# Kernel optimization log

Measured on AMD Instinct MI355X. Metric: run time of the kernel, lower is better.

The kernel has to match this reference:

```python
import jax, jax.numpy as jnp
import numpy as np
from math import sqrt

EPS = 1e-8


def setup_inputs() -> dict:
    rng = jax.random.key(0)
    k1, k2, k3 = jax.random.split(rng, 3)
    BS, NA, NB, NK, NV = 16, 2048, 2048, 64, 64
    key = jax.random.normal(k1, (BS, NA, 1, NK), dtype=jnp.float32)
    query = jax.random.normal(k2, (BS, 1, NB, NK), dtype=jnp.float32)
    value = jax.random.normal(k3, (BS, NA, NV), dtype=jnp.float32)
    return {"key": key, "query": query, "value": value}


def reference(key, query, value):
    # key: (BS, NA, 1, NK); query: (BS, 1, NB, NK); value: (BS, NA, NV)
    NK = key.shape[-1]
    NV = value.shape[-1]
    BS, NB = query.shape[0], query.shape[2]
    # weights = sum(key * query, 3) / sqrt(NK)  -> (BS, NA, NB), via einsum
    w = jnp.einsum('bak,bnk->ban', key[:, :, 0, :], query[:, 0, :, :]) / sqrt(NK)
    # softmax over NA (dim 1), beta=1, drop=False
    w = jax.nn.softmax(w, axis=1)
    # values = sum_a w[b,a,n] * value[b,a,v] -> (BS, NB, NV)
    vals = jnp.einsum('ban,bav->bnv', w, value)
    # norm over feature dim (torch.std is unbiased, ddof=1)
    v2 = vals.reshape(BS * NB, NV)
    mu = v2.mean(axis=1, keepdims=True)
    std = v2.std(axis=1, keepdims=True, ddof=1)
    v2 = (v2 - mu) / (std + EPS)
    out = v2.reshape(BS, NB, NV).transpose(0, 2, 1)  # (BS, NV, NB)
    return out, w
```

## Files before the change

kernel.cpp:

```cpp
#include <hip/hip_runtime.h>
#include <math.h>

#define BS 16
#define NA 2048
#define NB 2048
#define NK 64
#define NV 64
#define EPS 1e-8f

typedef float        f32x4  __attribute__((ext_vector_type(4)));
typedef __bf16       bf16x8 __attribute__((ext_vector_type(8)));
typedef short        s16x8  __attribute__((ext_vector_type(8)));
typedef unsigned int u32x4  __attribute__((ext_vector_type(4)));
typedef unsigned short u16x8 __attribute__((ext_vector_type(8)));

template <typename V>
__device__ __forceinline__ auto mfma_impl(V a, V b, f32x4 c, int)
    -> decltype(__builtin_amdgcn_mfma_f32_16x16x32_bf16(a, b, c, 0, 0, 0)) {
    return __builtin_amdgcn_mfma_f32_16x16x32_bf16(a, b, c, 0, 0, 0);
}
template <typename V>
__device__ __forceinline__ auto mfma_impl(V a, V b, f32x4 c, long)
    -> decltype(__builtin_amdgcn_mfma_f32_16x16x32_bf16(
           __builtin_bit_cast(s16x8, a), __builtin_bit_cast(s16x8, b), c, 0, 0, 0)) {
    return __builtin_amdgcn_mfma_f32_16x16x32_bf16(
        __builtin_bit_cast(s16x8, a), __builtin_bit_cast(s16x8, b), c, 0, 0, 0);
}
__device__ __forceinline__ f32x4 mfma_bf16(u32x4 a, u32x4 b, f32x4 c) {
    bf16x8 av = __builtin_bit_cast(bf16x8, a);
    bf16x8 bv = __builtin_bit_cast(bf16x8, b);
    return mfma_impl(av, bv, c, 0);
}

__device__ __forceinline__ unsigned short f2bf(float x) {
    unsigned u = __builtin_bit_cast(unsigned, x);
    unsigned r = (u + 0x7FFFu + ((u >> 16) & 1u)) >> 16;
    return (unsigned short)r;
}
__device__ __forceinline__ u16x8 pk8(f32x4 a, f32x4 b) {
    u16x8 p;
    p[0] = f2bf(a[0]); p[1] = f2bf(a[1]); p[2] = f2bf(a[2]); p[3] = f2bf(a[3]);
    p[4] = f2bf(b[0]); p[5] = f2bf(b[1]); p[6] = f2bf(b[2]); p[7] = f2bf(b[3]);
    return p;
}
__device__ __forceinline__ f32x4 ldg4(const float* p) { return *(const f32x4*)p; }

__device__ __forceinline__ void bar_lgkm() {
    asm volatile("s_waitcnt lgkmcnt(0)" ::: "memory");
    __builtin_amdgcn_s_barrier();
}

__device__ __forceinline__ int swz128(int lin) {
    const int r = lin >> 7;
    const int c16 = (lin >> 4) & 7;
    return (r << 7) + ((c16 ^ (r & 7)) << 4) + (lin & 15);
}

__global__ __launch_bounds__(256)
void conv_k_kernel(const float* __restrict__ key, unsigned short* __restrict__ kb) {
    size_t i = ((size_t)blockIdx.x * 256 + threadIdx.x) * 8;
    f32x4 a = *(const f32x4*)(key + i);
    f32x4 b = *(const f32x4*)(key + i + 4);
    *(u16x8*)(kb + i) = pk8(a, b);
}

__global__ __launch_bounds__(256)
void transpose_v_kernel(const float* __restrict__ v, unsigned short* __restrict__ vt) {
    __shared__ float tile[64][65];
    const int b = blockIdx.y, at = blockIdx.x * 64;
    const float* Vb = v + (size_t)b * NA * NV;
    unsigned short* Vtb = vt + (size_t)b * NV * NA;
    const int r = threadIdx.x >> 2, c = (threadIdx.x & 3) * 16;
    #pragma unroll
    for (int j = 0; j < 4; ++j)
        *(f32x4*)&tile[r][c + 4 * j] = ldg4(Vb + (size_t)(at + r) * NV + c + 4 * j);
    __syncthreads();
    u16x8 p0, p1;
    #pragma unroll
    for (int j = 0; j < 8; ++j) p0[j] = f2bf(tile[c + j][r]);
    #pragma unroll
    for (int j = 0; j < 8; ++j) p1[j] = f2bf(tile[c + 8 + j][r]);
    *(u16x8*)(Vtb + (size_t)r * NA + at + c) = p0;
    *(u16x8*)(Vtb + (size_t)r * NA + at + c + 8) = p1;
}

#define BN2 32
#define NT  32
#define KD0 0
#define KD1 8192
#define VD0 16384
#define VD1 24576
#define ESB 32768
#define LRED 36864
#define LINV 37376
#define SMEMSZ 37504

__global__ __launch_bounds__(256, 4)
void attn_main7_kernel(const unsigned short* __restrict__ kb,
                       const float* __restrict__ qf,
                       const unsigned short* __restrict__ vtb,
                       float* __restrict__ out,
                       float* __restrict__ wout)
{
    __shared__ __align__(16) char smem[SMEMSZ];
    const int tid = threadIdx.x, w = tid >> 6, lane = tid & 63;
    const int lr = lane & 15, lg = lane >> 4;

    const int lin = blockIdx.x;
    const int swz = (lin & 7) * 128 + (lin >> 3);
    const int b = swz >> 6, nb = (swz & 63) * BN2;

    const char* Kb = (const char*)(kb + (size_t)b * NA * NK);
    const char* Vt = (const char*)(vtb + (size_t)b * NV * NA);
    const float* Qb = qf + (size_t)b * NB * NK;
    float* Wb = wout + (size_t)b * NA * NB;
    float* Ob = out + (size_t)b * NV * NB;

    u32x4 af[2][2];
    #pragma unroll
    for (int t = 0; t < 2; ++t)
        #pragma unroll
        for (int c = 0; c < 2; ++c) {
            const float* qp = Qb + (size_t)(nb + t * 16 + lr) * NK + c * 32 + lg * 8;
            f32x4 qa = ldg4(qp);
            f32x4 qb2 = ldg4(qp + 4);
            af[t][c] = __builtin_bit_cast(u32x4, pk8(qa, qb2));
        }

    const int lin0 = tid * 16;
    const int lin1 = tid * 16 + 4096;
    const int kdst0 = swz128(lin0), kdst1 = swz128(lin1);
    const int vsrc0 = ((lin0 >> 7) * (NA * 2)) + (lin0 & 127);
    const int vsrc1 = ((lin1 >> 7) * (NA * 2)) + (lin1 & 127);

    const int row = w * 16 + lr;
    int kfro[2];
    #pragma unroll
    for (int c = 0; c < 2; ++c)
        kfro[c] = row * 128 + (((c * 4 + lg) ^ (row & 7)) << 4);
    int esro[2][2];
    #pragma unroll
    for (int t = 0; t < 2; ++t)
        #pragma unroll
        for (int c = 0; c < 2; ++c) {
            const int rr = t * 16 + lr;
            esro[t][c] = rr * 128 + (((c * 4 + lg) ^ (rr & 7)) << 4);
        }
    int eswo[2][4];
    #pragma unroll
    for (int t = 0; t < 2; ++t)
        #pragma unroll
        for (int r = 0; r < 4; ++r) {
            const int n = t * 16 + lg * 4 + r;
            eswo[t][r] = n * 128 + (((w * 2 + (lr >> 3)) ^ (n & 7)) << 4) + (lr & 7) * 2;
        }

    u32x4 kr0 = *(const u32x4*)(Kb + lin0);
    u32x4 kr1 = *(const u32x4*)(Kb + lin1);
    *(u32x4*)(smem + KD0 + kdst0) = kr0;
    *(u32x4*)(smem + KD0 + kdst1) = kr1;
    bar_lgkm();

    float lacc[2][4] = {};
    for (int i = 0; i < NT; ++i) {
        const int p = i & 1;
        if (i + 1 < NT) {
            kr0 = *(const u32x4*)(Kb + (i + 1) * 8192 + lin0);
            kr1 = *(const u32x4*)(Kb + (i + 1) * 8192 + lin1);
        }
        const char* kbuf = smem + (p ? KD1 : KD0);
        u32x4 kf0 = *(const u32x4*)(kbuf + kfro[0]);
        u32x4 kf1 = *(const u32x4*)(kbuf + kfro[1]);
        #pragma unroll
        for (int t = 0; t < 2; ++t) {
            f32x4 acc = {0.f, 0.f, 0.f, 0.f};
            acc = mfma_bf16(af[t][0], kf0, acc);
            acc = mfma_bf16(af[t][1], kf1, acc);
            #pragma unroll
            for (int r = 0; r < 4; ++r)
                lacc[t][r] += __expf(acc[r] * 0.125f);
        }
        if (i + 1 < NT) {
            char* kbn = smem + (p ? KD0 : KD1);
            *(u32x4*)(kbn + kdst0) = kr0;
            *(u32x4*)(kbn + kdst1) = kr1;
        }
        bar_lgkm();
    }

    #pragma unroll
    for (int t = 0; t < 2; ++t)
        #pragma unroll
        for (int r = 0; r < 4; ++r) {
            float v = lacc[t][r];
            v += __shfl_xor(v, 1); v += __shfl_xor(v, 2);
            v += __shfl_xor(v, 4); v += __shfl_xor(v, 8);
            lacc[t][r] = v;
        }
    if (lr == 0) {
        float* lp = (float*)(smem + LRED);
        #pragma unroll
        for (int t = 0; t < 2; ++t)
            #pragma unroll
            for (int r = 0; r < 4; ++r)
                lp[w * 32 + t * 16 + lg * 4 + r] = lacc[t][r];
    }
    __syncthreads();
    if (tid < 32) {
        const float* lp = (const float*)(smem + LRED);
        ((float*)(smem + LINV))[tid] =
            1.0f / (lp[tid] + lp[32 + tid] + lp[64 + tid] + lp[96 + tid]);
    }
    __syncthreads();
    f32x4 linv[2];
    linv[0] = *(const f32x4*)(smem + LINV + (lg * 4) * 4);
    linv[1] = *(const f32x4*)(smem + LINV + (16 + lg * 4) * 4);

    f32x4 pacc[2] = {{0.f,0.f,0.f,0.f},{0.f,0.f,0.f,0.f}};

    kr0 = *(const u32x4*)(Kb + lin0);
    kr1 = *(const u32x4*)(Kb + lin1);
    u32x4 vr0 = *(const u32x4*)(Vt + vsrc0);
    u32x4 vr1 = *(const u32x4*)(Vt + vsrc1);
    *(u32x4*)(smem + KD0 + kdst0) = kr0;
    *(u32x4*)(smem + KD0 + kdst1) = kr1;
    *(u32x4*)(smem + VD0 + kdst0) = vr0;
    *(u32x4*)(smem + VD0 + kdst1) = vr1;
    bar_lgkm();

    for (int i = 0; i < NT; ++i) {
        const int p = i & 1;
        if (i + 1 < NT) {
            kr0 = *(const u32x4*)(Kb + (i + 1) * 8192 + lin0);
            kr1 = *(const u32x4*)(Kb + (i + 1) * 8192 + lin1);
            vr0 = *(const u32x4*)(Vt + (i + 1) * 128 + vsrc0);
            vr1 = *(const u32x4*)(Vt + (i + 1) * 128 + vsrc1);
        }
        const char* kbuf = smem + (p ? KD1 : KD0);
        const char* vbuf = smem + (p ? VD1 : VD0);
        u32x4 kf0 = *(const u32x4*)(kbuf + kfro[0]);
        u32x4 kf1 = *(const u32x4*)(kbuf + kfro[1]);
        const int at = i * 64;
        #pragma unroll
        for (int t = 0; t < 2; ++t) {
            f32x4 acc = {0.f, 0.f, 0.f, 0.f};
            acc = mfma_bf16(af[t][0], kf0, acc);
            acc = mfma_bf16(af[t][1], kf1, acc);
            f32x4 wv;
            #pragma unroll
            for (int r = 0; r < 4; ++r)
                wv[r] = __expf(acc[r] * 0.125f) * linv[t][r];
            *(f32x4*)(Wb + (size_t)(at + row) * NB + nb + t * 16 + lg * 4) = wv;
            #pragma unroll
            for (int r = 0; r < 4; ++r)
                *(unsigned short*)(smem + ESB + eswo[t][r]) = f2bf(wv[r]);
        }
        bar_lgkm();

        u32x4 pa[2][2];
        #pragma unroll
        for (int t = 0; t < 2; ++t)
            #pragma unroll
            for (int c = 0; c < 2; ++c)
                pa[t][c] = *(const u32x4*)(smem + ESB + esro[t][c]);
        u32x4 vf0 = *(const u32x4*)(vbuf + kfro[0]);
        u32x4 vf1 = *(const u32x4*)(vbuf + kfro[1]);
        #pragma unroll
        for (int t = 0; t < 2; ++t) {
            pacc[t] = mfma_bf16(pa[t][0], vf0, pacc[t]);
            pacc[t] = mfma_bf16(pa[t][1], vf1, pacc[t]);
        }
        if (i + 1 < NT) {
            char* kbn = smem + (p ? KD0 : KD1);
            char* vbn = smem + (p ? VD0 : VD1);
            *(u32x4*)(kbn + kdst0) = kr0;
            *(u32x4*)(kbn + kdst1) = kr1;
            *(u32x4*)(vbn + kdst0) = vr0;
            *(u32x4*)(vbn + kdst1) = vr1;
        }
        bar_lgkm();
    }

    __syncthreads();
    float* vals = (float*)smem;
    #pragma unroll
    for (int t = 0; t < 2; ++t)
        #pragma unroll
        for (int r = 0; r < 4; ++r)
            vals[(t * 16 + lg * 4 + r) * 66 + w * 16 + lr] = pacc[t][r];
    __syncthreads();
    {
        const int n = tid >> 3, v0 = (tid & 7) * 8;
        float sv[8], s1 = 0.f, s2 = 0.f;
        #pragma unroll
        for (int j = 0; j < 8; ++j) {
            float x = vals[n * 66 + v0 + j];
            sv[j] = x; s1 += x; s2 = fmaf(x, x, s2);
        }
        s1 += __shfl_xor(s1, 1); s2 += __shfl_xor(s2, 1);
        s1 += __shfl_xor(s1, 2); s2 += __shfl_xor(s2, 2);
        s1 += __shfl_xor(s1, 4); s2 += __shfl_xor(s2, 4);
        const float mu = s1 * (1.0f / 64.0f);
        float var = (s2 - 64.0f * mu * mu) * (1.0f / 63.0f);
        var = fmaxf(var, 0.0f);
        const float istd = 1.0f / (sqrtf(var) + EPS);
        #pragma unroll
        for (int j = 0; j < 8; ++j)
            vals[n * 66 + v0 + j] = (sv[j] - mu) * istd;
    }
    __syncthreads();
    {
        const int v = tid >> 2, q = (tid & 3) * 8;
        f32x4 o0, o1;
        #pragma unroll
        for (int j = 0; j < 4; ++j) o0[j] = vals[(q + j) * 66 + v];
        #pragma unroll
        for (int j = 0; j < 4; ++j) o1[j] = vals[(q + 4 + j) * 66 + v];
        *(f32x4*)(Ob + (size_t)v * NB + nb + q) = o0;
        *(f32x4*)(Ob + (size_t)v * NB + nb + q + 4) = o1;
    }
}

#define SQ 72
#define OSTR 68
#define SMEM_BYTES 38144

__global__ __launch_bounds__(256, 2)
void attn_fb_kernel(const float* __restrict__ key, const float* __restrict__ query,
                    const float* __restrict__ value, float* __restrict__ out,
                    float* __restrict__ wout)
{
    __shared__ __align__(16) char smem[SMEM_BYTES];
    unsigned short* Qs = (unsigned short*)(smem);
    unsigned short* Ks = (unsigned short*)(smem + 9216);
    unsigned short* Vts = (unsigned short*)(smem + 18432);
    unsigned short* Es = (unsigned short*)(smem + 27648);
    float* linv_s = (float*)(smem + 36864);
    float (*lred)[64] = (float (*)[64])(smem + 37120);
    float* outl = (float*)(smem + 18432);

    const int tid = threadIdx.x, wave = tid >> 6, lane = tid & 63;
    const int lr = lane & 15, lg = lane >> 4;
    const int b = blockIdx.y, nb = blockIdx.x * 64, aw = wave * 16;

    const float* Kb = key + (size_t)b * NA * NK;
    const float* Qb = query + (size_t)b * NB * NK;
    const float* Vb = value + (size_t)b * NA * NV;
    float* Wb = wout + (size_t)b * NA * NB;
    float* Ob = out + (size_t)b * NV * NB;

    {
        const int r = tid >> 2, c = (tid & 3) * 16;
        const float* src = Qb + (size_t)(nb + r) * NK + c;
        f32x4 q0 = ldg4(src), q1 = ldg4(src + 4), q2 = ldg4(src + 8), q3 = ldg4(src + 12);
        *(u16x8*)&Qs[r * SQ + c] = pk8(q0, q1);
        *(u16x8*)&Qs[r * SQ + c + 8] = pk8(q2, q3);
    }
    float lacc[4][4] = {};
    for (int at = 0; at < NA; at += 64) {
        {
            const int r = tid >> 2, c = (tid & 3) * 16;
            const float* src = Kb + (size_t)(at + r) * NK + c;
            f32x4 k0 = ldg4(src), k1 = ldg4(src + 4), k2 = ldg4(src + 8), k3 = ldg4(src + 12);
            *(u16x8*)&Ks[r * SQ + c] = pk8(k0, k1);
            *(u16x8*)&Ks[r * SQ + c + 8] = pk8(k2, k3);
        }
        __syncthreads();
        u32x4 bf0 = *(const u32x4*)&Ks[(aw + lr) * SQ + (lg * 8)];
        u32x4 bf1 = *(const u32x4*)&Ks[(aw + lr) * SQ + (32 + lg * 8)];
        #pragma unroll
        for (int t = 0; t < 4; ++t) {
            f32x4 acc = {0.f, 0.f, 0.f, 0.f};
            u32x4 af0 = *(const u32x4*)&Qs[(t * 16 + lr) * SQ + (lg * 8)];
            u32x4 af1 = *(const u32x4*)&Qs[(t * 16 + lr) * SQ + (32 + lg * 8)];
            acc = mfma_bf16(af0, bf0, acc);
            acc = mfma_bf16(af1, bf1, acc);
            #pragma unroll
            for (int r = 0; r < 4; ++r) lacc[t][r] += __expf(acc[r] * 0.125f);
        }
        __syncthreads();
    }
    #pragma unroll
    for (int t = 0; t < 4; ++t)
        #pragma unroll
        for (int r = 0; r < 4; ++r) {
            float v = lacc[t][r];
            v += __shfl_xor(v, 1); v += __shfl_xor(v, 2);
            v += __shfl_xor(v, 4); v += __shfl_xor(v, 8);
            lacc[t][r] = v;
        }
    if (lr == 0)
        #pragma unroll
        for (int t = 0; t < 4; ++t)
            #pragma unroll
            for (int r = 0; r < 4; ++r)
                lred[wave][t * 16 + lg * 4 + r] = lacc[t][r];
    __syncthreads();
    if (tid < 64) {
        float s = lred[0][tid] + lred[1][tid] + lred[2][tid] + lred[3][tid];
        linv_s[tid] = 1.0f / s;
    }
    __syncthreads();
    f32x4 linv[4];
    #pragma unroll
    for (int t = 0; t < 4; ++t) linv[t] = *(const f32x4*)&linv_s[t * 16 + lg * 4];

    f32x4 pacc[4] = {{0.f,0.f,0.f,0.f},{0.f,0.f,0.f,0.f},{0.f,0.f,0.f,0.f},{0.f,0.f,0.f,0.f}};
    for (int at = 0; at < NA; at += 64) {
        {
            const int r = tid >> 2, c = (tid & 3) * 16;
            const float* src = Kb + (size_t)(at + r) * NK + c;
            f32x4 k0 = ldg4(src), k1 = ldg4(src + 4), k2 = ldg4(src + 8), k3 = ldg4(src + 12);
            *(u16x8*)&Ks[r * SQ + c] = pk8(k0, k1);
            *(u16x8*)&Ks[r * SQ + c + 8] = pk8(k2, k3);
        }
        {
            const int ap = (tid & 31) * 2, q = tid >> 5;
            const float* v0p = Vb + (size_t)(at + ap) * NV + q * 8;
            const float* v1p = v0p + NV;
            f32x4 a0 = ldg4(v0p), a1 = ldg4(v0p + 4);
            f32x4 b0 = ldg4(v1p), b1 = ldg4(v1p + 4);
            #pragma unroll
            for (int j = 0; j < 4; ++j) {
                unsigned int w0 = (unsigned)f2bf(a0[j]) | ((unsigned)f2bf(b0[j]) << 16);
                *(unsigned int*)&Vts[(q * 8 + j) * SQ + ap] = w0;
                unsigned int w1 = (unsigned)f2bf(a1[j]) | ((unsigned)f2bf(b1[j]) << 16);
                *(unsigned int*)&Vts[(q * 8 + 4 + j) * SQ + ap] = w1;
            }
        }
        __syncthreads();
        u32x4 bf0 = *(const u32x4*)&Ks[(aw + lr) * SQ + (lg * 8)];
        u32x4 bf1 = *(const u32x4*)&Ks[(aw + lr) * SQ + (32 + lg * 8)];
        #pragma unroll
        for (int t = 0; t < 4; ++t) {
            f32x4 acc = {0.f, 0.f, 0.f, 0.f};
            u32x4 af0 = *(const u32x4*)&Qs[(t * 16 + lr) * SQ + (lg * 8)];
            u32x4 af1 = *(const u32x4*)&Qs[(t * 16 + lr) * SQ + (32 + lg * 8)];
            acc = mfma_bf16(af0, bf0, acc);
            acc = mfma_bf16(af1, bf1, acc);
            f32x4 wv;
            #pragma unroll
            for (int r = 0; r < 4; ++r) wv[r] = __expf(acc[r] * 0.125f) * linv[t][r];
            *(f32x4*)(Wb + (size_t)(at + aw + lr) * NB + nb + t * 16 + lg * 4) = wv;
            #pragma unroll
            for (int r = 0; r < 4; ++r)
                Es[(t * 16 + lg * 4 + r) * SQ + (aw + lr)] = f2bf(wv[r]);
        }
        __syncthreads();
        u32x4 paf0 = *(const u32x4*)&Es[(wave * 16 + lr) * SQ + (lg * 8)];
        u32x4 paf1 = *(const u32x4*)&Es[(wave * 16 + lr) * SQ + (32 + lg * 8)];
        #pragma unroll
        for (int t = 0; t < 4; ++t) {
            u32x4 vb0 = *(const u32x4*)&Vts[(t * 16 + lr) * SQ + (lg * 8)];
            u32x4 vb1 = *(const u32x4*)&Vts[(t * 16 + lr) * SQ + (32 + lg * 8)];
            pacc[t] = mfma_bf16(paf0, vb0, pacc[t]);
            pacc[t] = mfma_bf16(paf1, vb1, pacc[t]);
        }
        __syncthreads();
    }
    float mu[4], istd[4];
    #pragma unroll
    for (int r = 0; r < 4; ++r) {
        float s1 = 0.f, s2 = 0.f;
        #pragma unroll
        for (int t = 0; t < 4; ++t) { float x = pacc[t][r]; s1 += x; s2 = fmaf(x, x, s2); }
        s1 += __shfl_xor(s1, 1); s2 += __shfl_xor(s2, 1);
        s1 += __shfl_xor(s1, 2); s2 += __shfl_xor(s2, 2);
        s1 += __shfl_xor(s1, 4); s2 += __shfl_xor(s2, 4);
        s1 += __shfl_xor(s1, 8); s2 += __shfl_xor(s2, 8);
        float m = s1 * (1.0f / 64.0f);
        float var = (s2 - 64.0f * m * m) * (1.0f / 63.0f);
        var = fmaxf(var, 0.0f);
        mu[r] = m; istd[r] = 1.0f / (sqrtf(var) + EPS);
    }
    #pragma unroll
    for (int t = 0; t < 4; ++t)
        #pragma unroll
        for (int r = 0; r < 4; ++r)
            outl[(t * 16 + lr) * OSTR + wave * 16 + lg * 4 + r] = (pacc[t][r] - mu[r]) * istd[r];
    __syncthreads();
    {
        const int v = tid >> 2, c = (tid & 3) * 16;
        float* dst = Ob + (size_t)v * NB + nb + c;
        const float* srcr = &outl[v * OSTR + c];
        #pragma unroll
        for (int j = 0; j < 4; ++j)
            *(f32x4*)(dst + 4 * j) = *(const f32x4*)(srcr + 4 * j);
    }
}

extern "C" void kernel_launch(void* const* d_in, const int* in_sizes, int n_in,
                              void* d_out, int out_size, void* d_ws, size_t ws_size,
                              hipStream_t stream) {
    const float* key   = (const float*)d_in[0];
    const float* query = (const float*)d_in[1];
    const float* value = (const float*)d_in[2];
    float* out  = (float*)d_out;
    float* wout = out + (size_t)BS * NV * NB;

    const size_t elems = (size_t)BS * NA * NK;
    const size_t need = 2 * elems * sizeof(unsigned short);
    if (ws_size >= need) {
        unsigned short* kbuf = (unsigned short*)d_ws;
        unsigned short* vt = kbuf + elems;
        conv_k_kernel<<<dim3((unsigned)(elems / (256 * 8))), 256, 0, stream>>>(key, kbuf);
        transpose_v_kernel<<<dim3(NA / 64, BS), 256, 0, stream>>>(value, vt);
        attn_main7_kernel<<<dim3(1024), 256, 0, stream>>>(kbuf, query, vt, out, wout);
    } else {
        attn_fb_kernel<<<dim3(NB / 64, BS), 256, 0, stream>>>(key, query, value, out, wout);
    }
}
```

Before: 91.76 us.

## Split softmax denominator pass into separate split-NA kernel with partial sums

Moves the first pass, which computes the exp-sum softmax denominator, out of the main attention kernel into a new lsum_kernel. The new kernel splits NA into 4 chunks across 4096 blocks and writes partial sums to workspace, and the main kernel then combines the four partials. The aim is more parallelism for the denominator pass, which at 1024 blocks each looping over all of NA underfilled the GPU. The cost is an extra kernel launch, a workspace round trip, and QK recomputation spread across more blocks.

```diff
diff --git a/kernel.cpp b/kernel.cpp
--- a/kernel.cpp
+++ b/kernel.cpp
@@ -85,6 +85,105 @@
 }
 
 #define BN2 32
+#define LKD0 0
+#define LKD1 8192
+#define LLRED 16384
+#define LSMEM 16896
+
+__global__ __launch_bounds__(256, 4)
+void lsum_kernel(const unsigned short* __restrict__ kb,
+                 const float* __restrict__ qf,
+                 float* __restrict__ lpart)
+{
+    __shared__ __align__(16) char smem[LSMEM];
+    const int tid = threadIdx.x, w = tid >> 6, lane = tid & 63;
+    const int lr = lane & 15, lg = lane >> 4;
+
+    const int lin = blockIdx.x;
+    const int swz = (lin & 7) * 512 + (lin >> 3);
+    const int b = swz >> 8, achunk = (swz >> 6) & 3, nb = (swz & 63) * BN2;
+
+    const char* Kc = (const char*)(kb + (size_t)b * NA * NK) + achunk * (512 * NK * 2);
+    const float* Qb = qf + (size_t)b * NB * NK;
+
+    u32x4 af[2][2];
+    #pragma unroll
+    for (int t = 0; t < 2; ++t)
+        #pragma unroll
+        for (int c = 0; c < 2; ++c) {
+            const float* qp = Qb + (size_t)(nb + t * 16 + lr) * NK + c * 32 + lg * 8;
+            f32x4 qa = ldg4(qp);
+            f32x4 qb2 = ldg4(qp + 4);
+            af[t][c] = __builtin_bit_cast(u32x4, pk8(qa, qb2));
+        }
+
+    const int lin0 = tid * 16;
+    const int lin1 = tid * 16 + 4096;
+    const int kdst0 = swz128(lin0), kdst1 = swz128(lin1);
+    const int row = w * 16 + lr;
+    int kfro[2];
+    #pragma unroll
+    for (int c = 0; c < 2; ++c)
+        kfro[c] = row * 128 + (((c * 4 + lg) ^ (row & 7)) << 4);
+
+    u32x4 kr0 = *(const u32x4*)(Kc + lin0);
+    u32x4 kr1 = *(const u32x4*)(Kc + lin1);
+    *(u32x4*)(smem + LKD0 + kdst0) = kr0;
+    *(u32x4*)(smem + LKD0 + kdst1) = kr1;
+    bar_lgkm();
+
+    float lacc[2][4] = {};
+    for (int i = 0; i < 8; ++i) {
+        const int p = i & 1;
+        if (i + 1 < 8) {
+            kr0 = *(const u32x4*)(Kc + (i + 1) * 8192 + lin0);
+            kr1 = *(const u32x4*)(Kc + (i + 1) * 8192 + lin1);
+        }
+        const char* kbuf = smem + (p ? LKD1 : LKD0);
+        u32x4 kf0 = *(const u32x4*)(kbuf + kfro[0]);
+        u32x4 kf1 = *(const u32x4*)(kbuf + kfro[1]);
+        #pragma unroll
+        for (int t = 0; t < 2; ++t) {
+            f32x4 acc = {0.f, 0.f, 0.f, 0.f};
+            acc = mfma_bf16(af[t][0], kf0, acc);
+            acc = mfma_bf16(af[t][1], kf1, acc);
+            #pragma unroll
+            for (int r = 0; r < 4; ++r)
+                lacc[t][r] += __expf(acc[r] * 0.125f);
+        }
+        if (i + 1 < 8) {
+            char* kbn = smem + (p ? LKD0 : LKD1);
+            *(u32x4*)(kbn + kdst0) = kr0;
+            *(u32x4*)(kbn + kdst1) = kr1;
+        }
+        bar_lgkm();
+    }
+
+    #pragma unroll
+    for (int t = 0; t < 2; ++t)
+        #pragma unroll
+        for (int r = 0; r < 4; ++r) {
+            float v = lacc[t][r];
+            v += __shfl_xor(v, 1); v += __shfl_xor(v, 2);
+            v += __shfl_xor(v, 4); v += __shfl_xor(v, 8);
+            lacc[t][r] = v;
+        }
+    if (lr == 0) {
+        float* lp = (float*)(smem + LLRED);
+        #pragma unroll
+        for (int t = 0; t < 2; ++t)
+            #pragma unroll
+            for (int r = 0; r < 4; ++r)
+                lp[w * 32 + t * 16 + lg * 4 + r] = lacc[t][r];
+    }
+    __syncthreads();
+    if (tid < 32) {
+        const float* lp = (const float*)(smem + LLRED);
+        lpart[((size_t)b * 4 + achunk) * NB + nb + tid] =
+            lp[tid] + lp[32 + tid] + lp[64 + tid] + lp[96 + tid];
+    }
+}
+
 #define NT  32
 #define KD0 0
 #define KD1 8192
@@ -96,9 +195,10 @@
 #define SMEMSZ 37504
 
 __global__ __launch_bounds__(256, 4)
-void attn_main7_kernel(const unsigned short* __restrict__ kb,
+void attn_main8_kernel(const unsigned short* __restrict__ kb,
                        const float* __restrict__ qf,
                        const unsigned short* __restrict__ vtb,
+                       const float* __restrict__ lpart,
                        float* __restrict__ out,
                        float* __restrict__ wout)
 {
@@ -127,6 +227,16 @@
             af[t][c] = __builtin_bit_cast(u32x4, pk8(qa, qb2));
         }
 
+    if (tid < 32) {
+        const float* lpb = lpart + (size_t)b * 4 * NB + nb;
+        float s = lpb[tid] + lpb[NB + tid] + lpb[2 * NB + tid] + lpb[3 * NB + tid];
+        ((float*)(smem + LINV))[tid] = 1.0f / s;
+    }
+    __syncthreads();
+    f32x4 linv[2];
+    linv[0] = *(const f32x4*)(smem + LINV + (lg * 4) * 4);
+    linv[1] = *(const f32x4*)(smem + LINV + (16 + lg * 4) * 4);
+
     const int lin0 = tid * 16;
     const int lin1 = tid * 16 + 4096;
     const int kdst0 = swz128(lin0), kdst1 = swz128(lin1);
@@ -155,71 +265,10 @@
             eswo[t][r] = n * 128 + (((w * 2 + (lr >> 3)) ^ (n & 7)) << 4) + (lr & 7) * 2;
         }
 
+    f32x4 pacc[2] = {{0.f,0.f,0.f,0.f},{0.f,0.f,0.f,0.f}};
+
     u32x4 kr0 = *(const u32x4*)(Kb + lin0);
     u32x4 kr1 = *(const u32x4*)(Kb + lin1);
-    *(u32x4*)(smem + KD0 + kdst0) = kr0;
-    *(u32x4*)(smem + KD0 + kdst1) = kr1;
-    bar_lgkm();
-
-    float lacc[2][4] = {};
-    for (int i = 0; i < NT; ++i) {
-        const int p = i & 1;
-        if (i + 1 < NT) {
-            kr0 = *(const u32x4*)(Kb + (i + 1) * 8192 + lin0);
-            kr1 = *(const u32x4*)(Kb + (i + 1) * 8192 + lin1);
-        }
-        const char* kbuf = smem + (p ? KD1 : KD0);
-        u32x4 kf0 = *(const u32x4*)(kbuf + kfro[0]);
-        u32x4 kf1 = *(const u32x4*)(kbuf + kfro[1]);
-        #pragma unroll
-        for (int t = 0; t < 2; ++t) {
-            f32x4 acc = {0.f, 0.f, 0.f, 0.f};
-            acc = mfma_bf16(af[t][0], kf0, acc);
-            acc = mfma_bf16(af[t][1], kf1, acc);
-            #pragma unroll
-            for (int r = 0; r < 4; ++r)
-                lacc[t][r] += __expf(acc[r] * 0.125f);
-        }
-        if (i + 1 < NT) {
-            char* kbn = smem + (p ? KD0 : KD1);
-            *(u32x4*)(kbn + kdst0) = kr0;
-            *(u32x4*)(kbn + kdst1) = kr1;
-        }
-        bar_lgkm();
-    }
-
-    #pragma unroll
-    for (int t = 0; t < 2; ++t)
-        #pragma unroll
-        for (int r = 0; r < 4; ++r) {
-            float v = lacc[t][r];
-            v += __shfl_xor(v, 1); v += __shfl_xor(v, 2);
-            v += __shfl_xor(v, 4); v += __shfl_xor(v, 8);
-            lacc[t][r] = v;
-        }
-    if (lr == 0) {
-        float* lp = (float*)(smem + LRED);
-        #pragma unroll
-        for (int t = 0; t < 2; ++t)
-            #pragma unroll
-            for (int r = 0; r < 4; ++r)
-                lp[w * 32 + t * 16 + lg * 4 + r] = lacc[t][r];
-    }
-    __syncthreads();
-    if (tid < 32) {
-        const float* lp = (const float*)(smem + LRED);
-        ((float*)(smem + LINV))[tid] =
-            1.0f / (lp[tid] + lp[32 + tid] + lp[64 + tid] + lp[96 + tid]);
-    }
-    __syncthreads();
-    f32x4 linv[2];
-    linv[0] = *(const f32x4*)(smem + LINV + (lg * 4) * 4);
-    linv[1] = *(const f32x4*)(smem + LINV + (16 + lg * 4) * 4);
-
-    f32x4 pacc[2] = {{0.f,0.f,0.f,0.f},{0.f,0.f,0.f,0.f}};
-
-    kr0 = *(const u32x4*)(Kb + lin0);
-    kr1 = *(const u32x4*)(Kb + lin1);
     u32x4 vr0 = *(const u32x4*)(Vt + vsrc0);
     u32x4 vr1 = *(const u32x4*)(Vt + vsrc1);
     *(u32x4*)(smem + KD0 + kdst0) = kr0;
@@ -499,13 +548,16 @@
     float* wout = out + (size_t)BS * NV * NB;
 
     const size_t elems = (size_t)BS * NA * NK;
-    const size_t need = 2 * elems * sizeof(unsigned short);
+    const size_t need = 2 * elems * sizeof(unsigned short)
+                      + (size_t)BS * 4 * NB * sizeof(float);
     if (ws_size >= need) {
         unsigned short* kbuf = (unsigned short*)d_ws;
         unsigned short* vt = kbuf + elems;
+        float* lpart = (float*)(vt + elems);
         conv_k_kernel<<<dim3((unsigned)(elems / (256 * 8))), 256, 0, stream>>>(key, kbuf);
         transpose_v_kernel<<<dim3(NA / 64, BS), 256, 0, stream>>>(value, vt);
-        attn_main7_kernel<<<dim3(1024), 256, 0, stream>>>(kbuf, query, vt, out, wout);
+        lsum_kernel<<<dim3(4096), 256, 0, stream>>>(kbuf, query, lpart);
+        attn_main8_kernel<<<dim3(1024), 256, 0, stream>>>(kbuf, query, vt, lpart, out, wout);
     } else {
         attn_fb_kernel<<<dim3(NB / 64, BS), 256, 0, stream>>>(key, query, value, out, wout);
     }
```

Measured after the change: 105.0 us. 1.14x slower.
